# Kernel optimization log

Hardware: AMD Instinct MI355X
Metric: run time of the kernel (lower is better)

## Reference

```python
import jax, jax.numpy as jnp
import numpy as np

S = 7          # grid cells per side (CFG['CELL_NUMS'])
L_COORD = 5.0  # CFG['L_COORD']
L_NOOBJ = 0.5  # CFG['L_NOOBJ']
N_BATCH = 16384


def setup_inputs() -> dict:
    key = jax.random.key(0)
    k1, k2, k3 = jax.random.split(key, 3)
    pred = jax.random.uniform(k1, (N_BATCH, S, S, 30), dtype=jnp.float32)
    target = jax.random.uniform(k2, (N_BATCH, S, S, 30), dtype=jnp.float32)
    obj = jax.random.uniform(k3, (N_BATCH, S, S)) < 0.3
    target = target.at[..., 4].set(jnp.where(obj, target[..., 4], 0.0))
    target = target.at[..., 9].set(jnp.where(obj, target[..., 9], 0.0))
    return {"pred_tensor": pred, "target_tensor": target}


def _yolo_v1_loss(pred, target):
    # pred/target: [N, S, S, 30] = [2 boxes x (x,y,w,h,c), 20 class probs]
    N = pred.shape[0]
    coo_f = (target[..., 4] > 0).astype(pred.dtype)   # [N,S,S] object cells
    noo_f = 1.0 - coo_f                                # no-object cells

    # no-object loss: confidence channels 4 and 9 on noo cells (sum-MSE)
    nooobj_loss = jnp.sum(
        noo_f * ((pred[..., 4] - target[..., 4]) ** 2
                 + (pred[..., 9] - target[..., 9]) ** 2))

    # class loss over object cells (sum-MSE over 20 classes)
    class_loss = jnp.sum(coo_f[..., None] * (pred[..., 10:] - target[..., 10:]) ** 2)

    # boxes: [N,S,S,2,5]
    pb = pred[..., :10].reshape(N, S, S, 2, 5)
    tb = target[..., :10].reshape(N, S, S, 2, 5)

    # xywh -> xyxy for the 2 predicted boxes and the first target box per cell
    p_lt = pb[..., :2] - 0.5 * pb[..., 2:4]
    p_rb = pb[..., :2] + 0.5 * pb[..., 2:4]
    t0 = tb[..., 0, :]                                 # target box used for IOU
    t_lt = t0[..., :2] - 0.5 * t0[..., 2:4]
    t_rb = t0[..., :2] + 0.5 * t0[..., 2:4]

    # NOTE: faithful reproduction of the source's compute_iou, including its
    # bug: wh = (rb - lt < 0).float(), so 'inter' is an indicator product.
    lt = jnp.maximum(p_lt, t_lt[..., None, :])         # [N,S,S,2,2]
    rb = jnp.minimum(p_rb, t_rb[..., None, :])
    wh_ind = (rb - lt < 0).astype(pred.dtype)
    inter = wh_ind[..., 0] * wh_ind[..., 1]            # [N,S,S,2]
    area1 = (p_rb[..., 0] - p_lt[..., 0]) * (p_rb[..., 1] - p_lt[..., 1])
    area2 = ((t_rb[..., 0] - t_lt[..., 0]) * (t_rb[..., 1] - t_lt[..., 1]))[..., None]
    iou = inter / (area1 + area2 - inter)              # [N,S,S,2]

    # responsible box = argmax IOU over the 2 predicted boxes per cell
    idx = jnp.argmax(iou, axis=-1)                     # [N,S,S]
    gather = idx[..., None, None]                      # [N,S,S,1,1]
    resp_p = jnp.take_along_axis(pb, gather, axis=3)[..., 0, :]  # [N,S,S,5]
    resp_t = jnp.take_along_axis(tb, gather, axis=3)[..., 0, :]

    contain_loss = jnp.sum(coo_f * (resp_p[..., 4] - resp_t[..., 4]) ** 2)

    # guard sqrt at masked-out cells so 0*d(sqrt(0)) does not produce NaN grads
    safe = coo_f[..., None] > 0
    sqrt_wp = jnp.sqrt(jnp.where(safe, resp_p[..., 2:4], 1.0))
    sqrt_wt = jnp.sqrt(jnp.where(safe, resp_t[..., 2:4], 1.0))
    loc_loss = (jnp.sum(coo_f[..., None] * (resp_p[..., :2] - resp_t[..., :2]) ** 2)
                + jnp.sum(coo_f[..., None] * (sqrt_wp - sqrt_wt) ** 2))

    return (L_COORD * loc_loss + contain_loss + L_NOOBJ * nooobj_loss + class_loss) / N


def reference(pred_tensor, target_tensor):
    return _yolo_v1_loss(pred_tensor, target_tensor)
```

## Files before the change

### kernel.cpp

```cpp
#include <hip/hip_runtime.h>


#define CH 30
#define CPW 32
#define WAVES 4
#define T 256
#define CPB (CPW * WAVES)
#define WREG_F (CPW * CH * 2)
#define INPUT_F (CPW * CH)

typedef __attribute__((address_space(3))) void* lds_vp;
typedef const __attribute__((address_space(1))) void* gvp;

__global__ __launch_bounds__(T, 5)
void yolo_partial(const float* __restrict__ pred,
                  const float* __restrict__ targ,
                  float* __restrict__ partial) {
    __shared__ float tile[WAVES * WREG_F];
    __shared__ float wave_sums[WAVES];

    const int tid = threadIdx.x;
    const int wave = tid >> 6;
    const int lane = tid & 63;

    float* wreg = &tile[wave * WREG_F];
    const long long cell0 = (long long)blockIdx.x * CPB + wave * CPW;
    const float* gt = targ + cell0 * CH;
    const float* gp = pred + cell0 * CH;

#pragma unroll
    for (int k = 0; k < 3; ++k) {
        const int idx = k * 64 + lane;
        __builtin_amdgcn_global_load_lds((gvp)(gt + idx * 4),
                                         (lds_vp)(wreg + idx * 4), 16, 0, 0);
        __builtin_amdgcn_global_load_lds((gvp)(gp + idx * 4),
                                         (lds_vp)(wreg + INPUT_F + idx * 4), 16, 0, 0);
    }
    if (lane < 48) {
        const int idx = 192 + lane;
        __builtin_amdgcn_global_load_lds((gvp)(gt + idx * 4),
                                         (lds_vp)(wreg + idx * 4), 16, 0, 0);
        __builtin_amdgcn_global_load_lds((gvp)(gp + idx * 4),
                                         (lds_vp)(wreg + INPUT_F + idx * 4), 16, 0, 0);
    }

    asm volatile("s_waitcnt vmcnt(0)" ::: "memory");

    float sum = 0.0f;
    if (lane < CPW) {
        const float2* t2 = (const float2*)(wreg + lane * CH);
        const float2* p2 = (const float2*)(wreg + INPUT_F + lane * CH);

        const float2 t01 = t2[0], t23 = t2[1], t45 = t2[2], t67 = t2[3], t89 = t2[4];
        const float2 p01 = p2[0], p23 = p2[1], p45 = p2[2], p67 = p2[3], p89 = p2[4];

        const float t4 = t45.x, t9 = t89.y;
        const bool coo = t4 > 0.0f;

        const float d4 = p45.x - t4;
        const float d9 = p89.y - t9;
        sum = coo ? 0.0f : 0.5f * (d4 * d4 + d9 * d9);

        if (coo) {
            float cl = 0.0f;
#pragma unroll
            for (int k = 0; k < 10; ++k) {
                const float2 pc = p2[5 + k];
                const float2 tc = t2[5 + k];
                const float dx = pc.x - tc.x;
                const float dy = pc.y - tc.y;
                cl += dx * dx + dy * dy;
            }
            sum += cl;

            const float tltx = t01.x - 0.5f * t23.x;
            const float tlty = t01.y - 0.5f * t23.y;
            const float trbx = t01.x + 0.5f * t23.x;
            const float trby = t01.y + 0.5f * t23.y;
            const float area2 = (trbx - tltx) * (trby - tlty);

            const float b0x = p01.x, b0y = p01.y, b0w = p23.x, b0h = p23.y;
            const float b1x = p45.y, b1y = p67.x, b1w = p67.y, b1h = p89.x;

            float iou0, iou1;
            {
                const float pltx = b0x - 0.5f * b0w, plty = b0y - 0.5f * b0h;
                const float prbx = b0x + 0.5f * b0w, prby = b0y + 0.5f * b0h;
                const float ltx = fmaxf(pltx, tltx), lty = fmaxf(plty, tlty);
                const float rbx = fminf(prbx, trbx), rby = fminf(prby, trby);
                const float inter = ((rbx - ltx < 0.0f) ? 1.0f : 0.0f) *
                                    ((rby - lty < 0.0f) ? 1.0f : 0.0f);
                const float area1 = (prbx - pltx) * (prby - plty);
                iou0 = inter / (area1 + area2 - inter);
            }
            {
                const float pltx = b1x - 0.5f * b1w, plty = b1y - 0.5f * b1h;
                const float prbx = b1x + 0.5f * b1w, prby = b1y + 0.5f * b1h;
                const float ltx = fmaxf(pltx, tltx), lty = fmaxf(plty, tlty);
                const float rbx = fminf(prbx, trbx), rby = fminf(prby, trby);
                const float inter = ((rbx - ltx < 0.0f) ? 1.0f : 0.0f) *
                                    ((rby - lty < 0.0f) ? 1.0f : 0.0f);
                const float area1 = (prbx - pltx) * (prby - plty);
                iou1 = inter / (area1 + area2 - inter);
            }
            const bool idx1 = iou1 > iou0;

            const float rpx = idx1 ? b1x : b0x;
            const float rpy = idx1 ? b1y : b0y;
            const float rpw = idx1 ? b1w : b0w;
            const float rph = idx1 ? b1h : b0h;
            const float rpc = idx1 ? p89.y : p45.x;
            const float rtx = idx1 ? t45.y : t01.x;
            const float rty = idx1 ? t67.x : t01.y;
            const float rtw = idx1 ? t67.y : t23.x;
            const float rth = idx1 ? t89.x : t23.y;
            const float rtc = idx1 ? t89.y : t45.x;

            const float dc = rpc - rtc;
            sum += dc * dc;

            const float dx = rpx - rtx;
            const float dy = rpy - rty;
            const float dw = sqrtf(rpw) - sqrtf(rtw);
            const float dh = sqrtf(rph) - sqrtf(rth);
            sum += 5.0f * (dx * dx + dy * dy + dw * dw + dh * dh);
        }
    }

#pragma unroll
    for (int off = 32; off > 0; off >>= 1)
        sum += __shfl_down(sum, off, 64);
    if (lane == 0) wave_sums[wave] = sum;
    __syncthreads();
    if (tid == 0) {
        float tot = 0.0f;
#pragma unroll
        for (int w = 0; w < WAVES; ++w) tot += wave_sums[w];
        partial[blockIdx.x] = tot;
    }
}

__global__ __launch_bounds__(256)
void yolo_reduce(const float* __restrict__ partial, int n, float* __restrict__ out) {
    __shared__ float wave_sums[4];
    float s = 0.0f;
    const int n4 = n >> 2;
    const float4* p4 = (const float4*)partial;
    for (int v = threadIdx.x; v < n4; v += 256) {
        const float4 x = p4[v];
        s += (x.x + x.y) + (x.z + x.w);
    }
    for (int v = (n4 << 2) + threadIdx.x; v < n; v += 256)
        s += partial[v];
#pragma unroll
    for (int off = 32; off > 0; off >>= 1)
        s += __shfl_down(s, off, 64);
    const int wave = threadIdx.x >> 6;
    const int lane = threadIdx.x & 63;
    if (lane == 0) wave_sums[wave] = s;
    __syncthreads();
    if (threadIdx.x == 0) {
        const float tot = wave_sums[0] + wave_sums[1] + wave_sums[2] + wave_sums[3];
        out[0] = tot * (1.0f / 16384.0f);
    }
}

extern "C" void kernel_launch(void* const* d_in, const int* in_sizes, int n_in,
                              void* d_out, int out_size, void* d_ws, size_t ws_size,
                              hipStream_t stream) {
    const float* pred = (const float*)d_in[0];
    const float* targ = (const float*)d_in[1];
    float* out = (float*)d_out;
    float* partial = (float*)d_ws;

    const int n_cells = in_sizes[0] / CH;
    const int blocks = n_cells / CPB;

    yolo_partial<<<blocks, T, 0, stream>>>(pred, targ, partial);
    yolo_reduce<<<1, 256, 0, stream>>>(partial, blocks, out);
}
```

Before: 204.7 us.

## Replace LDS staging with direct per-thread loads over a grid-stride, double-buffered cell loop

Drops the global_load_lds staging tile. Each thread now reads its cells directly into registers as float2 and handles about four cells spaced LANES_TOTAL apart. Two register buffers are used so the next cell's loads can be issued while the current cell is computed. The grid is fixed at 768 blocks and the cell count is hardcoded, so other input sizes are not supported. Per-thread strided 120-byte loads are uncoalesced across lanes and raise register pressure.

```diff
diff --git a/kernel.cpp b/kernel.cpp
--- a/kernel.cpp
+++ b/kernel.cpp
@@ -2,141 +2,136 @@
 
 
 #define CH 30
-#define CPW 32
-#define WAVES 4
-#define T 256
-#define CPB (CPW * WAVES)
-#define WREG_F (CPW * CH * 2)
-#define INPUT_F (CPW * CH)
+#define LANES_TOTAL 196608
+#define N_CELLS 802816
 
-typedef __attribute__((address_space(3))) void* lds_vp;
-typedef const __attribute__((address_space(1))) void* gvp;
+struct Cell {
+    float2 t[15];
+    float2 p[15];
+};
 
-__global__ __launch_bounds__(T, 5)
+__device__ __forceinline__ void load_cell(Cell& c,
+                                          const float* __restrict__ targ,
+                                          const float* __restrict__ pred,
+                                          long long cell) {
+    const float2* tb = (const float2*)targ + cell * 15;
+    const float2* pb = (const float2*)pred + cell * 15;
+#pragma unroll
+    for (int i = 0; i < 15; ++i) c.t[i] = tb[i];
+#pragma unroll
+    for (int i = 0; i < 15; ++i) c.p[i] = pb[i];
+}
+
+__device__ __forceinline__ float cell_loss(const Cell& c) {
+    const float2 t01 = c.t[0], t23 = c.t[1], t45 = c.t[2], t67 = c.t[3], t89 = c.t[4];
+    const float2 p01 = c.p[0], p23 = c.p[1], p45 = c.p[2], p67 = c.p[3], p89 = c.p[4];
+
+    const float t4 = t45.x;
+    const bool coo = t4 > 0.0f;
+
+    const float d4 = p45.x - t4;
+    const float d9 = p89.y - t89.y;
+    float sum = coo ? 0.0f : 0.5f * (d4 * d4 + d9 * d9);
+
+    if (coo) {
+        float cl = 0.0f;
+#pragma unroll
+        for (int k = 0; k < 10; ++k) {
+            const float dx = c.p[5 + k].x - c.t[5 + k].x;
+            const float dy = c.p[5 + k].y - c.t[5 + k].y;
+            cl += dx * dx + dy * dy;
+        }
+        sum += cl;
+
+        const float tltx = t01.x - 0.5f * t23.x;
+        const float tlty = t01.y - 0.5f * t23.y;
+        const float trbx = t01.x + 0.5f * t23.x;
+        const float trby = t01.y + 0.5f * t23.y;
+        const float area2 = (trbx - tltx) * (trby - tlty);
+
+        const float b0x = p01.x, b0y = p01.y, b0w = p23.x, b0h = p23.y;
+        const float b1x = p45.y, b1y = p67.x, b1w = p67.y, b1h = p89.x;
+
+        float iou0, iou1;
+        {
+            const float pltx = b0x - 0.5f * b0w, plty = b0y - 0.5f * b0h;
+            const float prbx = b0x + 0.5f * b0w, prby = b0y + 0.5f * b0h;
+            const float ltx = fmaxf(pltx, tltx), lty = fmaxf(plty, tlty);
+            const float rbx = fminf(prbx, trbx), rby = fminf(prby, trby);
+            const float inter = ((rbx - ltx < 0.0f) ? 1.0f : 0.0f) *
+                                ((rby - lty < 0.0f) ? 1.0f : 0.0f);
+            const float area1 = (prbx - pltx) * (prby - plty);
+            iou0 = inter / (area1 + area2 - inter);
+        }
+        {
+            const float pltx = b1x - 0.5f * b1w, plty = b1y - 0.5f * b1h;
+            const float prbx = b1x + 0.5f * b1w, prby = b1y + 0.5f * b1h;
+            const float ltx = fmaxf(pltx, tltx), lty = fmaxf(plty, tlty);
+            const float rbx = fminf(prbx, trbx), rby = fminf(prby, trby);
+            const float inter = ((rbx - ltx < 0.0f) ? 1.0f : 0.0f) *
+                                ((rby - lty < 0.0f) ? 1.0f : 0.0f);
+            const float area1 = (prbx - pltx) * (prby - plty);
+            iou1 = inter / (area1 + area2 - inter);
+        }
+        const bool idx1 = iou1 > iou0;
+
+        const float rpx = idx1 ? b1x : b0x;
+        const float rpy = idx1 ? b1y : b0y;
+        const float rpw = idx1 ? b1w : b0w;
+        const float rph = idx1 ? b1h : b0h;
+        const float rpc = idx1 ? p89.y : p45.x;
+        const float rtx = idx1 ? t45.y : t01.x;
+        const float rty = idx1 ? t67.x : t01.y;
+        const float rtw = idx1 ? t67.y : t23.x;
+        const float rth = idx1 ? t89.x : t23.y;
+        const float rtc = idx1 ? t89.y : t45.x;
+
+        const float dc = rpc - rtc;
+        sum += dc * dc;
+
+        const float dx = rpx - rtx;
+        const float dy = rpy - rty;
+        const float dw = sqrtf(rpw) - sqrtf(rtw);
+        const float dh = sqrtf(rph) - sqrtf(rth);
+        sum += 5.0f * (dx * dx + dy * dy + dw * dw + dh * dh);
+    }
+    return sum;
+}
+
+__global__ __launch_bounds__(256, 3)
 void yolo_partial(const float* __restrict__ pred,
                   const float* __restrict__ targ,
                   float* __restrict__ partial) {
-    __shared__ float tile[WAVES * WREG_F];
-    __shared__ float wave_sums[WAVES];
+    __shared__ float wave_sums[4];
 
     const int tid = threadIdx.x;
-    const int wave = tid >> 6;
-    const int lane = tid & 63;
+    const long long gid = (long long)blockIdx.x * 256 + tid;
+    const bool extra = gid < (N_CELLS - 4 * (long long)LANES_TOTAL);
 
-    float* wreg = &tile[wave * WREG_F];
-    const long long cell0 = (long long)blockIdx.x * CPB + wave * CPW;
-    const float* gt = targ + cell0 * CH;
-    const float* gp = pred + cell0 * CH;
+    Cell A, B;
+    float sum = 0.0f;
 
-#pragma unroll
-    for (int k = 0; k < 3; ++k) {
-        const int idx = k * 64 + lane;
-        __builtin_amdgcn_global_load_lds((gvp)(gt + idx * 4),
-                                         (lds_vp)(wreg + idx * 4), 16, 0, 0);
-        __builtin_amdgcn_global_load_lds((gvp)(gp + idx * 4),
-                                         (lds_vp)(wreg + INPUT_F + idx * 4), 16, 0, 0);
-    }
-    if (lane < 48) {
-        const int idx = 192 + lane;
-        __builtin_amdgcn_global_load_lds((gvp)(gt + idx * 4),
-                                         (lds_vp)(wreg + idx * 4), 16, 0, 0);
-        __builtin_amdgcn_global_load_lds((gvp)(gp + idx * 4),
-                                         (lds_vp)(wreg + INPUT_F + idx * 4), 16, 0, 0);
-    }
-
-    asm volatile("s_waitcnt vmcnt(0)" ::: "memory");
-
-    float sum = 0.0f;
-    if (lane < CPW) {
-        const float2* t2 = (const float2*)(wreg + lane * CH);
-        const float2* p2 = (const float2*)(wreg + INPUT_F + lane * CH);
-
-        const float2 t01 = t2[0], t23 = t2[1], t45 = t2[2], t67 = t2[3], t89 = t2[4];
-        const float2 p01 = p2[0], p23 = p2[1], p45 = p2[2], p67 = p2[3], p89 = p2[4];
-
-        const float t4 = t45.x, t9 = t89.y;
-        const bool coo = t4 > 0.0f;
-
-        const float d4 = p45.x - t4;
-        const float d9 = p89.y - t9;
-        sum = coo ? 0.0f : 0.5f * (d4 * d4 + d9 * d9);
-
-        if (coo) {
-            float cl = 0.0f;
-#pragma unroll
-            for (int k = 0; k < 10; ++k) {
-                const float2 pc = p2[5 + k];
-                const float2 tc = t2[5 + k];
-                const float dx = pc.x - tc.x;
-                const float dy = pc.y - tc.y;
-                cl += dx * dx + dy * dy;
-            }
-            sum += cl;
-
-            const float tltx = t01.x - 0.5f * t23.x;
-            const float tlty = t01.y - 0.5f * t23.y;
-            const float trbx = t01.x + 0.5f * t23.x;
-            const float trby = t01.y + 0.5f * t23.y;
-            const float area2 = (trbx - tltx) * (trby - tlty);
-
-            const float b0x = p01.x, b0y = p01.y, b0w = p23.x, b0h = p23.y;
-            const float b1x = p45.y, b1y = p67.x, b1w = p67.y, b1h = p89.x;
-
-            float iou0, iou1;
-            {
-                const float pltx = b0x - 0.5f * b0w, plty = b0y - 0.5f * b0h;
-                const float prbx = b0x + 0.5f * b0w, prby = b0y + 0.5f * b0h;
-                const float ltx = fmaxf(pltx, tltx), lty = fmaxf(plty, tlty);
-                const float rbx = fminf(prbx, trbx), rby = fminf(prby, trby);
-                const float inter = ((rbx - ltx < 0.0f) ? 1.0f : 0.0f) *
-                                    ((rby - lty < 0.0f) ? 1.0f : 0.0f);
-                const float area1 = (prbx - pltx) * (prby - plty);
-                iou0 = inter / (area1 + area2 - inter);
-            }
-            {
-                const float pltx = b1x - 0.5f * b1w, plty = b1y - 0.5f * b1h;
-                const float prbx = b1x + 0.5f * b1w, prby = b1y + 0.5f * b1h;
-                const float ltx = fmaxf(pltx, tltx), lty = fmaxf(plty, tlty);
-                const float rbx = fminf(prbx, trbx), rby = fminf(prby, trby);
-                const float inter = ((rbx - ltx < 0.0f) ? 1.0f : 0.0f) *
-                                    ((rby - lty < 0.0f) ? 1.0f : 0.0f);
-                const float area1 = (prbx - pltx) * (prby - plty);
-                iou1 = inter / (area1 + area2 - inter);
-            }
-            const bool idx1 = iou1 > iou0;
-
-            const float rpx = idx1 ? b1x : b0x;
-            const float rpy = idx1 ? b1y : b0y;
-            const float rpw = idx1 ? b1w : b0w;
-            const float rph = idx1 ? b1h : b0h;
-            const float rpc = idx1 ? p89.y : p45.x;
-            const float rtx = idx1 ? t45.y : t01.x;
-            const float rty = idx1 ? t67.x : t01.y;
-            const float rtw = idx1 ? t67.y : t23.x;
-            const float rth = idx1 ? t89.x : t23.y;
-            const float rtc = idx1 ? t89.y : t45.x;
-
-            const float dc = rpc - rtc;
-            sum += dc * dc;
-
-            const float dx = rpx - rtx;
-            const float dy = rpy - rty;
-            const float dw = sqrtf(rpw) - sqrtf(rtw);
-            const float dh = sqrtf(rph) - sqrtf(rth);
-            sum += 5.0f * (dx * dx + dy * dy + dw * dw + dh * dh);
-        }
-    }
+    load_cell(A, targ, pred, gid);
+    load_cell(B, targ, pred, gid + LANES_TOTAL);
+    sum += cell_loss(A);
+    load_cell(A, targ, pred, gid + 2LL * LANES_TOTAL);
+    sum += cell_loss(B);
+    load_cell(B, targ, pred, gid + 3LL * LANES_TOTAL);
+    sum += cell_loss(A);
+    if (extra) load_cell(A, targ, pred, gid + 4LL * LANES_TOTAL);
+    sum += cell_loss(B);
+    if (extra) sum += cell_loss(A);
 
 #pragma unroll
     for (int off = 32; off > 0; off >>= 1)
         sum += __shfl_down(sum, off, 64);
+    const int wave = tid >> 6;
+    const int lane = tid & 63;
     if (lane == 0) wave_sums[wave] = sum;
     __syncthreads();
     if (tid == 0) {
-        float tot = 0.0f;
-#pragma unroll
-        for (int w = 0; w < WAVES; ++w) tot += wave_sums[w];
-        partial[blockIdx.x] = tot;
+        partial[blockIdx.x] = (wave_sums[0] + wave_sums[1]) +
+                              (wave_sums[2] + wave_sums[3]);
     }
 }
 
@@ -173,9 +168,8 @@
     float* out = (float*)d_out;
     float* partial = (float*)d_ws;
 
-    const int n_cells = in_sizes[0] / CH;
-    const int blocks = n_cells / CPB;
+    const int blocks = LANES_TOTAL / 256;
 
-    yolo_partial<<<blocks, T, 0, stream>>>(pred, targ, partial);
+    yolo_partial<<<blocks, 256, 0, stream>>>(pred, targ, partial);
     yolo_reduce<<<1, 256, 0, stream>>>(partial, blocks, out);
 }
```

Result: no change. 208.5 us (+1.8%).
